# Performance work log

Hardware: AMD Instinct MI355X
Metric: run time of the kernel (lower is better)

## Reference

```python
import jax, jax.numpy as jnp
import numpy as np


def setup_inputs() -> dict:
    key = jax.random.key(0)
    B, F, D = 16384, 26, 32
    inputs = jax.random.normal(key, (B, F, D), dtype=jnp.float32)
    return {"inputs": inputs}


def reference(inputs) -> jnp.ndarray:
    # inputs: [B, F, D]. Output: [B, F*(F-1)/2, D] of pairwise elementwise products,
    # ordered as (i, j) with i < j, i outer loop, j inner loop (matches tf double loop).
    F = inputs.shape[1]
    i_idx, j_idx = np.triu_indices(F, k=1)  # row-major order == original loop order
    # Single fused gather-multiply over index pairs.
    return inputs[:, i_idx, :] * inputs[:, j_idx, :]
```

## Files before the change

kernel.cpp:

```cpp
#include <hip/hip_runtime.h>

#define NF 26
#define ND 32
#define NPAIR 325
#define ROW_F4 (NF * ND / 4)
#define OUT_F4 (NPAIR * ND / 4)
#define ROWS 4
#define NTHREADS 256
#define KFULL (OUT_F4 / NTHREADS)
#define KTAIL (OUT_F4 % NTHREADS)

typedef float f32x4 __attribute__((ext_vector_type(4)));

struct PairTab { unsigned short v[NPAIR]; };
constexpr PairTab make_tab() {
    PairTab t{};
    int n = 0;
    for (int i = 0; i < NF; ++i)
        for (int j = i + 1; j < NF; ++j)
            t.v[n++] = (unsigned short)((i * (ND / 4)) | ((j * (ND / 4)) << 8));
    return t;
}
__constant__ PairTab c_tab = make_tab();

__global__ __launch_bounds__(NTHREADS) void interaction_kernel(
    const f32x4* __restrict__ in, f32x4* __restrict__ out)
{
    __shared__ f32x4 s_row[ROWS * ROW_F4];

    const int b0  = blockIdx.x * ROWS;
    const int tid = threadIdx.x;

    const f32x4* src = in + (size_t)b0 * ROW_F4;
    for (int t = tid; t < ROWS * ROW_F4; t += NTHREADS)
        s_row[t] = src[t];

    int aoff[KFULL + 1], boff[KFULL + 1];
    #pragma unroll
    for (int k = 0; k <= KFULL; ++k) {
        const int q = (k < KFULL) ? (tid + k * NTHREADS)
                                  : (KFULL * NTHREADS + (tid < KTAIL ? tid : 0));
        const unsigned int t = c_tab.v[q >> 3];
        const int d = q & 7;
        aoff[k] = (int)(t & 0xffu) + d;
        boff[k] = (int)(t >> 8) + d;
    }

    __syncthreads();

    #pragma unroll 1
    for (int r = 0; r < ROWS; ++r) {
        const f32x4* __restrict__ row = s_row + r * ROW_F4;
        f32x4* __restrict__ dst = out + (size_t)(b0 + r) * OUT_F4;
        #pragma unroll
        for (int k = 0; k < KFULL; ++k) {
            const f32x4 a = row[aoff[k]];
            const f32x4 v = row[boff[k]];
            const f32x4 rr = a * v;
            __builtin_nontemporal_store(rr, dst + tid + k * NTHREADS);
        }
        if (tid < KTAIL) {
            const f32x4 a = row[aoff[KFULL]];
            const f32x4 v = row[boff[KFULL]];
            const f32x4 rr = a * v;
            __builtin_nontemporal_store(rr, dst + KFULL * NTHREADS + tid);
        }
    }
}

extern "C" void kernel_launch(void* const* d_in, const int* in_sizes, int n_in,
                              void* d_out, int out_size, void* d_ws, size_t ws_size,
                              hipStream_t stream) {
    const f32x4* in  = (const f32x4*)d_in[0];
    f32x4*       out = (f32x4*)d_out;
    const int B = in_sizes[0] / (NF * ND);
    interaction_kernel<<<B / ROWS, NTHREADS, 0, stream>>>(in, out);
}
```

Before: 141.6 us.

## Process multiple row groups per block with register prefetch and double-buffered LDS

Each block now handles four groups of four batch rows instead of one. While the current group is computed from shared memory, the next group's input is loaded into registers and then written to the other shared buffer. This hides the input load latency and amortizes the per-block setup of pair offsets. In exchange the grid is four times smaller and each group adds two barriers, which can reduce the number of blocks resident on each compute unit.

```diff
diff --git a/kernel.cpp b/kernel.cpp
--- a/kernel.cpp
+++ b/kernel.cpp
@@ -6,6 +6,8 @@
 #define ROW_F4 (NF * ND / 4)
 #define OUT_F4 (NPAIR * ND / 4)
 #define ROWS 4
+#define GROUPS_PER_BLOCK 4
+#define GROUP_F4 (ROWS * ROW_F4)
 #define NTHREADS 256
 #define KFULL (OUT_F4 / NTHREADS)
 #define KTAIL (OUT_F4 % NTHREADS)
@@ -26,14 +28,10 @@
 __global__ __launch_bounds__(NTHREADS) void interaction_kernel(
     const f32x4* __restrict__ in, f32x4* __restrict__ out)
 {
-    __shared__ f32x4 s_row[ROWS * ROW_F4];
+    __shared__ f32x4 s[2][GROUP_F4];
 
-    const int b0  = blockIdx.x * ROWS;
     const int tid = threadIdx.x;
-
-    const f32x4* src = in + (size_t)b0 * ROW_F4;
-    for (int t = tid; t < ROWS * ROW_F4; t += NTHREADS)
-        s_row[t] = src[t];
+    const long g0 = (long)blockIdx.x * GROUPS_PER_BLOCK;
 
     int aoff[KFULL + 1], boff[KFULL + 1];
     #pragma unroll
@@ -46,24 +44,51 @@
         boff[k] = (int)(t >> 8) + d;
     }
 
+    {
+        const f32x4* __restrict__ src = in + g0 * GROUP_F4;
+        #pragma unroll
+        for (int k = 0; k < 3; ++k) s[0][tid + k * NTHREADS] = src[tid + k * NTHREADS];
+        if (tid < GROUP_F4 - 3 * NTHREADS) s[0][tid + 3 * NTHREADS] = src[tid + 3 * NTHREADS];
+    }
     __syncthreads();
 
     #pragma unroll 1
-    for (int r = 0; r < ROWS; ++r) {
-        const f32x4* __restrict__ row = s_row + r * ROW_F4;
-        f32x4* __restrict__ dst = out + (size_t)(b0 + r) * OUT_F4;
-        #pragma unroll
-        for (int k = 0; k < KFULL; ++k) {
-            const f32x4 a = row[aoff[k]];
-            const f32x4 v = row[boff[k]];
-            const f32x4 rr = a * v;
-            __builtin_nontemporal_store(rr, dst + tid + k * NTHREADS);
+    for (int g = 0; g < GROUPS_PER_BLOCK; ++g) {
+        const int p = g & 1;
+        const bool has_next = (g + 1 < GROUPS_PER_BLOCK);
+
+        f32x4 pf0, pf1, pf2, pf3;
+        if (has_next) {
+            const f32x4* __restrict__ src = in + (g0 + g + 1) * GROUP_F4;
+            pf0 = src[tid];
+            pf1 = src[tid + NTHREADS];
+            pf2 = src[tid + 2 * NTHREADS];
+            if (tid < GROUP_F4 - 3 * NTHREADS) pf3 = src[tid + 3 * NTHREADS];
         }
-        if (tid < KTAIL) {
-            const f32x4 a = row[aoff[KFULL]];
-            const f32x4 v = row[boff[KFULL]];
-            const f32x4 rr = a * v;
-            __builtin_nontemporal_store(rr, dst + KFULL * NTHREADS + tid);
+
+        const long baseRow = (g0 + g) * ROWS;
+        #pragma unroll 1
+        for (int r = 0; r < ROWS; ++r) {
+            const f32x4* __restrict__ row = &s[p][r * ROW_F4];
+            f32x4* __restrict__ dst = out + (baseRow + r) * OUT_F4;
+            #pragma unroll
+            for (int k = 0; k < KFULL; ++k) {
+                const f32x4 rr = row[aoff[k]] * row[boff[k]];
+                __builtin_nontemporal_store(rr, dst + tid + k * NTHREADS);
+            }
+            if (tid < KTAIL) {
+                const f32x4 rr = row[aoff[KFULL]] * row[boff[KFULL]];
+                __builtin_nontemporal_store(rr, dst + KFULL * NTHREADS + tid);
+            }
+        }
+
+        if (has_next) {
+            __syncthreads();
+            s[1 - p][tid] = pf0;
+            s[1 - p][tid + NTHREADS] = pf1;
+            s[1 - p][tid + 2 * NTHREADS] = pf2;
+            if (tid < GROUP_F4 - 3 * NTHREADS) s[1 - p][tid + 3 * NTHREADS] = pf3;
+            __syncthreads();
         }
     }
 }
@@ -74,5 +99,6 @@
     const f32x4* in  = (const f32x4*)d_in[0];
     f32x4*       out = (f32x4*)d_out;
     const int B = in_sizes[0] / (NF * ND);
-    interaction_kernel<<<B / ROWS, NTHREADS, 0, stream>>>(in, out);
+    const int blocks = B / (ROWS * GROUPS_PER_BLOCK);
+    interaction_kernel<<<blocks, NTHREADS, 0, stream>>>(in, out);
 }
```

New measurement: 147.8 us. +4.4%, slower.
